# Performance work log

Hardware: AMD Instinct MI355X
Metric: run time of the kernel (lower is better)

## Reference

```python
import jax, jax.numpy as jnp
import numpy as np

N, D, K, P, A = 16384, 256, 32, 64, 5
H, KD, NPT, FACT = 8, 32, 8, 2
RBF_BINS, RBF_MAX, REL_CLIP = 16, 10.0, 32


def _norm(v, eps=1e-6):
    return v * jax.lax.rsqrt(jnp.square(v).sum(-1, keepdims=True) + eps)


def extract_frames(pos):
    # pos: [N, A, 3]; backbone atoms 0=N, 1=CA, 2=C (Gram-Schmidt AF-style frame)
    n, ca, c = pos[:, 0], pos[:, 1], pos[:, 2]
    e1 = _norm(c - ca)
    u = n - ca
    e2 = _norm(u - (u * e1).sum(-1, keepdims=True) * e1)
    e3 = jnp.cross(e1, e2)
    R = jnp.stack([e1, e2, e3], axis=-1)  # [N,3,3], columns = frame axes
    t = ca
    local = jnp.einsum('nji,naj->nai', R, pos - t[:, None])  # R^T (p - t)
    return R, t, local


def distance_rbf(d):
    centers = jnp.linspace(0.0, RBF_MAX, RBF_BINS)
    sigma = RBF_MAX / RBF_BINS
    return jnp.exp(-jnp.square((d[..., None] - centers) / sigma))


def layer_norm(x, scale, offset, eps=1e-5):
    mu = x.mean(-1, keepdims=True)
    var = jnp.square(x - mu).mean(-1, keepdims=True)
    return (x - mu) * jax.lax.rsqrt(var + eps) * scale + offset


def setup_inputs() -> dict:
    key = jax.random.key(0)
    ks = jax.random.split(key, 20)
    f32 = jnp.float32
    rnd = lambda i, shape, s=0.02: jax.random.normal(ks[i], shape, f32) * s
    inp = {}
    inp['local'] = jax.random.normal(ks[0], (N, D), f32)
    inp['pos'] = jax.random.normal(ks[1], (N, A, 3), f32) * 3.0
    inp['neighbours'] = jax.random.randint(ks[2], (N, K), 0, N, jnp.int32)
    inp['resi'] = jnp.arange(N, dtype=jnp.int32) % 512
    inp['chain'] = jnp.arange(N, dtype=jnp.int32) // 2048
    inp['batch'] = jnp.arange(N, dtype=jnp.int32) // 4096
    inp['update_mask'] = jnp.ones((N, 1), bool)
    inp['mask'] = jnp.ones((N,), bool)
    FIN = A * 3 + A * RBF_BINS
    FPAIR = A * 3 + A * RBF_BINS + (2 * REL_CLIP + 1) + 2
    FOUT = H * KD + H * P + H * NPT * 3 + H * NPT
    inp['w_in'] = rnd(3, (FIN, D))
    inp['w_pair'] = rnd(4, (FPAIR, P))
    inp['b_pair'] = jnp.zeros((P,), f32)
    inp['ln1_s'] = jnp.ones((D,), f32); inp['ln1_o'] = jnp.zeros((D,), f32)
    inp['wq'] = rnd(5, (D, H * KD)); inp['wk'] = rnd(6, (D, H * KD)); inp['wv'] = rnd(7, (D, H * KD))
    inp['wqp'] = rnd(8, (D, H * NPT * 3)); inp['wkp'] = rnd(9, (D, H * NPT * 3)); inp['wvp'] = rnd(10, (D, H * NPT * 3))
    inp['wb'] = rnd(11, (P, H))
    inp['gamma'] = jnp.ones((H,), f32)
    inp['wo'] = rnd(12, (FOUT, D)); inp['bo'] = jnp.zeros((D,), f32)
    inp['ln2_s'] = jnp.ones((D,), f32); inp['ln2_o'] = jnp.zeros((D,), f32)
    DH = D * FACT
    inp['wg'] = rnd(13, (D, DH)); inp['wvm'] = rnd(14, (D, DH)); inp['wom'] = rnd(15, (DH, D))
    inp['ln3_s'] = jnp.ones((D,), f32); inp['ln3_o'] = jnp.zeros((D,), f32)
    inp['wpos'] = rnd(16, (D, A * 3))
    return inp


def reference(local, pos, w_in, w_pair, b_pair, ln1_s, ln1_o, wq, wk, wv, wqp, wkp, wvp,
              wb, gamma, wo, bo, ln2_s, ln2_o, wg, wvm, wom, ln3_s, ln3_o, wpos,
              neighbours, resi, chain, batch, update_mask, mask):
    n_res = local.shape[0]
    kk = neighbours.shape[1]
    R, t, local_pos = extract_frames(pos)  # [N,3,3], [N,3], [N,A,3]
    # --- geometric input features ---
    dloc = jnp.sqrt(jnp.square(local_pos).sum(-1) + 1e-12)
    feat = jnp.concatenate([_norm(local_pos).reshape(n_res, -1),
                            distance_rbf(dloc).reshape(n_res, -1)], axis=-1)
    local = local + feat @ w_in
    # --- pair features over kNN edges ---
    idx = jnp.clip(neighbours, 0, n_res - 1)
    pos_j = pos[idx]  # [N,K,A,3]
    rel = jnp.einsum('nji,nkaj->nkai', R, pos_j - t[:, None, None])  # neighbour atoms in frame i
    dij = jnp.sqrt(jnp.square(rel).sum(-1) + 1e-12)  # [N,K,A]
    dirs = rel / (dij[..., None] + 1e-6)
    rp = jnp.clip(resi[idx] - resi[:, None], -REL_CLIP, REL_CLIP) + REL_CLIP
    rp_oh = jax.nn.one_hot(rp, 2 * REL_CLIP + 1, dtype=local.dtype)
    same_chain = (chain[idx] == chain[:, None])[..., None].astype(local.dtype)
    same_batch = (batch[idx] == batch[:, None])[..., None].astype(local.dtype)
    pf = jnp.concatenate([dirs.reshape(n_res, kk, -1), distance_rbf(dij).reshape(n_res, kk, -1),
                          rp_oh, same_chain, same_batch], axis=-1)
    pair = jax.nn.gelu(pf @ w_pair + b_pair)  # [N,K,P]
    pair_mask = mask[:, None] & mask[idx] & (neighbours >= 0) & (batch[idx] == batch[:, None])
    # --- sparse invariant point attention ---
    x = layer_norm(local, ln1_s, ln1_o)
    q = (x @ wq).reshape(n_res, H, KD)
    k = (x @ wk).reshape(n_res, H, KD)
    v = (x @ wv).reshape(n_res, H, KD)
    to_glob = lambda pts: jnp.einsum('nij,nhpj->nhpi', R, pts) + t[:, None, None]
    qp = to_glob((x @ wqp).reshape(n_res, H, NPT, 3))
    kp = to_glob((x @ wkp).reshape(n_res, H, NPT, 3))
    vp = to_glob((x @ wvp).reshape(n_res, H, NPT, 3))
    qk = jnp.einsum('nhd,nkhd->nkh', q, k[idx]) / np.float32(np.sqrt(KD))
    d2 = jnp.square(qp[:, None] - kp[idx]).sum(-1).sum(-1)  # [N,K,H]
    wc = np.float32(np.sqrt(2.0 / (9.0 * NPT)))
    wl = np.float32(np.sqrt(1.0 / 3.0))
    logits = wl * (qk + pair @ wb - 0.5 * wc * jax.nn.softplus(gamma) * d2)
    logits = jnp.where(pair_mask[..., None], logits, -1e9)
    att = jax.nn.softmax(logits, axis=1)
    att = jnp.where(pair_mask[..., None], att, 0.0)
    o_s = jnp.einsum('nkh,nkhd->nhd', att, v[idx]).reshape(n_res, -1)
    o_pt = jnp.einsum('nkh,nkhpi->nhpi', att, vp[idx])
    o_pt = jnp.einsum('nji,nhpj->nhpi', R, o_pt - t[:, None, None])  # back to local frame
    o_n = jnp.sqrt(jnp.square(o_pt).sum(-1) + 1e-8)
    o_pr = jnp.einsum('nkh,nkc->nhc', att, pair).reshape(n_res, -1)
    ipa = jnp.concatenate([o_s, o_pr, o_pt.reshape(n_res, -1), o_n.reshape(n_res, -1)], -1) @ wo + bo
    local = local + ipa
    # --- gated MLP ---
    x = layer_norm(local, ln2_s, ln2_o)
    local = local + (jax.nn.gelu(x @ wg) * (x @ wvm)) @ wom
    # --- equivariant position update (scale = 1.0) ---
    x = layer_norm(local, ln3_s, ln3_o)
    new_lp = local_pos + (x @ wpos).reshape(n_res, A, 3)
    new_pos = jnp.einsum('nij,naj->nai', R, new_lp) + t[:, None]
    pos = jnp.where(update_mask[..., None], new_pos, pos)
    return local, pos
```

## Files before the change

### kernel.cpp

```cpp
#include <hip/hip_runtime.h>
#include <hip/hip_bf16.h>
#include <math.h>

#define DMODEL 256
#define KNB 32
#define NHEAD 8
#define FIN 95
#define FPD 95
#define KPAD 104
#define FOUT 1024
#define DHID 512

typedef __hip_bfloat16 bf16;
typedef __attribute__((ext_vector_type(8))) short short8;
typedef __attribute__((ext_vector_type(4))) float floatx4;

__device__ inline float B2F(bf16 x) { return __bfloat162float(x); }
__device__ inline bf16 F2B(float x) { return __float2bfloat16(x); }
__device__ inline unsigned short f2bs(float x) {
    bf16 h = __float2bfloat16(x);
    return *reinterpret_cast<unsigned short*>(&h);
}
__device__ inline float bs2f(short s) {
    return __uint_as_float(((unsigned)(unsigned short)s) << 16);
}

__device__ inline float gelu_t(float x) {
    return 0.5f * x * (1.f + tanhf(0.7978845608028654f * (x + 0.044715f * x * x * x)));
}

#define OFF_WALL 0
#define OFF_WO   344064
#define OFF_WG   606208
#define OFF_WVM  737280
#define OFF_WOM  868352
#define OFF_WP   999424
#define OFF_WIN  1006080
#define WT_TOTAL 1032704

__global__ __launch_bounds__(256) void kT(const float* __restrict__ wq, const float* __restrict__ wk,
                                          const float* __restrict__ wv, const float* __restrict__ wqp,
                                          const float* __restrict__ wkp, const float* __restrict__ wvp,
                                          const float* __restrict__ wo, const float* __restrict__ wg,
                                          const float* __restrict__ wvm, const float* __restrict__ wom,
                                          const float* __restrict__ w_pair, const float* __restrict__ w_in,
                                          unsigned short* __restrict__ wt) {
    int stride = gridDim.x * 256;
    for (int e = blockIdx.x * 256 + threadIdx.x; e < WT_TOTAL; e += stride) {
        float v;
        if (e < OFF_WO) {
            int n = e >> 8, k = e & 255;
            if (n < 256) v = wq[k * 256 + n];
            else if (n < 512) v = wk[k * 256 + n - 256];
            else if (n < 768) v = wv[k * 256 + n - 512];
            else if (n < 960) v = wqp[k * 192 + n - 768];
            else if (n < 1152) v = wkp[k * 192 + n - 960];
            else v = wvp[k * 192 + n - 1152];
        } else if (e < OFF_WG) {
            int u = e - OFF_WO; int n = u >> 10, k = u & 1023;
            v = wo[k * 256 + n];
        } else if (e < OFF_WVM) {
            int u = e - OFF_WG; int n = u >> 8, k = u & 255;
            v = wg[k * 512 + n];
        } else if (e < OFF_WOM) {
            int u = e - OFF_WVM; int n = u >> 8, k = u & 255;
            v = wvm[k * 512 + n];
        } else if (e < OFF_WP) {
            int u = e - OFF_WOM; int n = u >> 9, k = u & 511;
            v = wom[k * 256 + n];
        } else if (e < OFF_WIN) {
            int u = e - OFF_WP; int n = u / KPAD, k = u % KPAD;
            v = (k < FPD) ? w_pair[k * 64 + n] : 0.f;
        } else {
            int u = e - OFF_WIN; int n = u / KPAD, k = u % KPAD;
            v = (k < FIN) ? w_in[k * 256 + n] : 0.f;
        }
        wt[e] = f2bs(v);
    }
}

__global__ __launch_bounds__(256) void kA1(const float* __restrict__ pos,
                                           float* __restrict__ Rw,
                                           float* __restrict__ lpw,
                                           unsigned short* __restrict__ featb) {
    int tid = threadIdx.x;
    int res = tid >> 5, lt = tid & 31;
    int ri = blockIdx.x * 8 + res;
    const float* pp = pos + (size_t)ri * 15;
    float nx = pp[0], ny = pp[1], nz = pp[2];
    float cax = pp[3], cay = pp[4], caz = pp[5];
    float cx = pp[6], cy = pp[7], cz = pp[8];
    float e1x = cx - cax, e1y = cy - cay, e1z = cz - caz;
    float inv = rsqrtf(e1x * e1x + e1y * e1y + e1z * e1z + 1e-6f);
    e1x *= inv; e1y *= inv; e1z *= inv;
    float ux = nx - cax, uy = ny - cay, uz = nz - caz;
    float d = ux * e1x + uy * e1y + uz * e1z;
    float wx = ux - d * e1x, wy = uy - d * e1y, wz = uz - d * e1z;
    inv = rsqrtf(wx * wx + wy * wy + wz * wz + 1e-6f);
    float e2x = wx * inv, e2y = wy * inv, e2z = wz * inv;
    float e3x = e1y * e2z - e1z * e2y;
    float e3y = e1z * e2x - e1x * e2z;
    float e3z = e1x * e2y - e1y * e2x;
    float R[9] = {e1x, e2x, e3x, e1y, e2y, e3y, e1z, e2z, e3z};

    __shared__ float lpS[8][15];
    __shared__ float ddS[8][5], dinvS[8][5];

    if (lt < 9) Rw[(size_t)ri * 9 + lt] = R[lt];
    if (lt < 15) {
        int a = lt / 3, ii = lt % 3;
        float px = pp[a * 3 + 0] - cax, py = pp[a * 3 + 1] - cay, pz = pp[a * 3 + 2] - caz;
        float v = R[0 * 3 + ii] * px + R[1 * 3 + ii] * py + R[2 * 3 + ii] * pz;
        lpS[res][lt] = v;
        lpw[(size_t)ri * 15 + lt] = v;
    }
    __syncthreads();
    if (lt < 5) {
        float s = lpS[res][lt * 3] * lpS[res][lt * 3] + lpS[res][lt * 3 + 1] * lpS[res][lt * 3 + 1] +
                  lpS[res][lt * 3 + 2] * lpS[res][lt * 3 + 2];
        ddS[res][lt] = sqrtf(s + 1e-12f);
        dinvS[res][lt] = rsqrtf(s + 1e-6f);
    }
    __syncthreads();
    for (int e = lt; e < KPAD; e += 32) {
        float v;
        if (e < 15) v = lpS[res][e] * dinvS[res][e / 3];
        else if (e < 95) {
            int u = e - 15, a = u >> 4, b = u & 15;
            float z = (ddS[res][a] - (float)b * (10.f / 15.f)) * (1.f / 0.625f);
            v = expf(-z * z);
        } else v = 0.f;
        featb[(size_t)ri * KPAD + e] = f2bs(v);
    }
}

__global__ __launch_bounds__(256) void kB(const float* __restrict__ local,
                                          const unsigned short* __restrict__ featb,
                                          const float* __restrict__ ln1_s,
                                          const float* __restrict__ ln1_o,
                                          const unsigned short* __restrict__ wAllT,
                                          const unsigned short* __restrict__ w_inT,
                                          float* __restrict__ dlocal,
                                          bf16* __restrict__ qbh, bf16* __restrict__ kbh,
                                          bf16* __restrict__ vbh, bf16* __restrict__ qpl,
                                          bf16* __restrict__ kpl, bf16* __restrict__ vpl) {
    int r0 = blockIdx.x * 32;
    int tid = threadIdx.x;
    __shared__ __align__(16) unsigned short featA[32 * KPAD];
    __shared__ __align__(16) unsigned short xbf[32 * 264];
    __shared__ float statsS[32 * 4];

    {
        const short8* src = reinterpret_cast<const short8*>(featb + (size_t)r0 * KPAD);
        short8* dst = reinterpret_cast<short8*>(featA);
        for (int c = tid; c < 32 * KPAD / 8; c += 256) dst[c] = src[c];
    }
    __syncthreads();

    int lane = tid & 63, w = tid >> 6;
    int mtile = w & 1, par = w >> 1;
    int m = lane & 15, quad = lane >> 4;

    short8 fa[3];
#pragma unroll
    for (int ks = 0; ks < 3; ks++)
        fa[ks] = *reinterpret_cast<const short8*>(&featA[(mtile * 16 + m) * KPAD + ks * 32 + quad * 8]);
    float lupv[8][4];
#pragma unroll
    for (int j = 0; j < 8; j++) {
        int nt = par + 2 * j;
        floatx4 c = {0.f, 0.f, 0.f, 0.f};
        const short8* bp = reinterpret_cast<const short8*>(w_inT + (size_t)(nt * 16 + m) * KPAD);
#pragma unroll
        for (int ks = 0; ks < 3; ks++)
            c = __builtin_amdgcn_mfma_f32_16x16x32_bf16(fa[ks], bp[ks * 4 + quad], c, 0, 0, 0);
        int col = nt * 16 + m;
#pragma unroll
        for (int r = 0; r < 4; r++) {
            int row = mtile * 16 + quad * 4 + r;
            float lv = local[(size_t)(r0 + row) * 256 + col] + c[r];
            lupv[j][r] = lv;
            dlocal[(size_t)(r0 + row) * 256 + col] = lv;
        }
    }
    {
        float s[4] = {0.f, 0.f, 0.f, 0.f}, ss[4] = {0.f, 0.f, 0.f, 0.f};
#pragma unroll
        for (int j = 0; j < 8; j++)
#pragma unroll
            for (int r = 0; r < 4; r++) { s[r] += lupv[j][r]; ss[r] += lupv[j][r] * lupv[j][r]; }
#pragma unroll
        for (int mask = 1; mask < 16; mask <<= 1)
#pragma unroll
            for (int r = 0; r < 4; r++) { s[r] += __shfl_xor(s[r], mask); ss[r] += __shfl_xor(ss[r], mask); }
        if (m == 0) {
#pragma unroll
            for (int r = 0; r < 4; r++) {
                int row = mtile * 16 + quad * 4 + r;
                statsS[row * 4 + par * 2 + 0] = s[r];
                statsS[row * 4 + par * 2 + 1] = ss[r];
            }
        }
    }
    __syncthreads();
    {
        float mu[4], rs_[4];
#pragma unroll
        for (int r = 0; r < 4; r++) {
            int row = mtile * 16 + quad * 4 + r;
            float S = statsS[row * 4 + 0] + statsS[row * 4 + 2];
            float SS = statsS[row * 4 + 1] + statsS[row * 4 + 3];
            float m_ = S * (1.f / 256.f);
            mu[r] = m_;
            rs_[r] = rsqrtf(SS * (1.f / 256.f) - m_ * m_ + 1e-5f);
        }
#pragma unroll
        for (int j = 0; j < 8; j++) {
            int col = (par + 2 * j) * 16 + m;
            float g = ln1_s[col], o = ln1_o[col];
#pragma unroll
            for (int r = 0; r < 4; r++) {
                int row = mtile * 16 + quad * 4 + r;
                xbf[row * 264 + col] = f2bs((lupv[j][r] - mu[r]) * rs_[r] * g + o);
            }
        }
    }
    __syncthreads();

    short8 afr[8];
#pragma unroll
    for (int ks = 0; ks < 8; ks++)
        afr[ks] = *reinterpret_cast<const short8*>(&xbf[(mtile * 16 + m) * 264 + ks * 32 + quad * 8]);
    for (int nt = par; nt < 84; nt += 2) {
        floatx4 c = {0.f, 0.f, 0.f, 0.f};
        const short8* bp = reinterpret_cast<const short8*>(wAllT + (size_t)(nt * 16 + m) * 256);
#pragma unroll
        for (int ks = 0; ks < 8; ks++)
            c = __builtin_amdgcn_mfma_f32_16x16x32_bf16(afr[ks], bp[ks * 4 + quad], c, 0, 0, 0);
        int colg = nt * 16 + m;
        bf16* O; int c0, ncol;
        if (colg < 256)       { O = qbh; c0 = colg;        ncol = 256; }
        else if (colg < 512)  { O = kbh; c0 = colg - 256;  ncol = 256; }
        else if (colg < 768)  { O = vbh; c0 = colg - 512;  ncol = 256; }
        else if (colg < 960)  { O = qpl; c0 = colg - 768;  ncol = 192; }
        else if (colg < 1152) { O = kpl; c0 = colg - 960;  ncol = 192; }
        else                  { O = vpl; c0 = colg - 1152; ncol = 192; }
#pragma unroll
        for (int r = 0; r < 4; r++) {
            int rg = r0 + mtile * 16 + quad * 4 + r;
            O[(size_t)rg * ncol + c0] = F2B(c[r]);
        }
    }
}

__global__ __launch_bounds__(256) void kP(const bf16* __restrict__ qpl,
                                          const bf16* __restrict__ kpl,
                                          const bf16* __restrict__ vpl,
                                          const float* __restrict__ Rw,
                                          const float* __restrict__ pos,
                                          float* __restrict__ qpg,
                                          float* __restrict__ kpg,
                                          float* __restrict__ vpg) {
    int r0 = blockIdx.x * 4;
    int tid = threadIdx.x;
    for (int u = tid; u < 4 * 192; u += 256) {
        int r = u / 192, e = u % 192, hp = e / 3, ii = e % 3;
        int ri = r0 + r;
        float R0 = Rw[(size_t)ri * 9 + ii * 3 + 0];
        float R1 = Rw[(size_t)ri * 9 + ii * 3 + 1];
        float R2 = Rw[(size_t)ri * 9 + ii * 3 + 2];
        float tt = pos[(size_t)ri * 15 + 3 + ii];
        size_t base = (size_t)ri * 192 + hp * 3;
        qpg[(size_t)ri * 192 + e] = R0 * B2F(qpl[base]) + R1 * B2F(qpl[base + 1]) + R2 * B2F(qpl[base + 2]) + tt;
        kpg[(size_t)ri * 192 + e] = R0 * B2F(kpl[base]) + R1 * B2F(kpl[base + 1]) + R2 * B2F(kpl[base + 2]) + tt;
        vpg[(size_t)ri * 192 + e] = R0 * B2F(vpl[base]) + R1 * B2F(vpl[base + 1]) + R2 * B2F(vpl[base + 2]) + tt;
    }
}

__global__ __launch_bounds__(256) void kC(const float* __restrict__ pos,
                                          const int* __restrict__ nbr,
                                          const int* __restrict__ resi,
                                          const int* __restrict__ chain,
                                          const int* __restrict__ batch,
                                          const int* __restrict__ mask,
                                          const float* __restrict__ Rw,
                                          const float* __restrict__ w_pair,
                                          const unsigned short* __restrict__ wT,
                                          const float* __restrict__ b_pair,
                                          const float* __restrict__ wbm,
                                          const float* __restrict__ gamma,
                                          const bf16* __restrict__ qbh,
                                          const bf16* __restrict__ kbh,
                                          const bf16* __restrict__ vbh,
                                          const float* __restrict__ qpg,
                                          const float* __restrict__ kpg,
                                          const float* __restrict__ vpg,
                                          bf16* __restrict__ ipab,
                                          int N) {
    int i = blockIdx.x;
    int tid = threadIdx.x;
    __shared__ __align__(16) float qS[256];
    __shared__ __align__(16) float qpS[192];
    __shared__ __align__(16) unsigned short pfA[KNB * KPAD];
    __shared__ __align__(16) float pairS[KNB][68];
    __shared__ __align__(16) float wbmS[NHEAD][68];
    __shared__ float lg[KNB * NHEAD];
    __shared__ float optg[192];
    __shared__ float ipaS[FOUT];
    __shared__ int idxS[KNB], rpS[KNB], scS[KNB], sbS[KNB], pmS[KNB];

    float R[9];
#pragma unroll
    for (int u = 0; u < 9; u++) R[u] = Rw[(size_t)i * 9 + u];
    float t0 = pos[(size_t)i * 15 + 3];
    float t1 = pos[(size_t)i * 15 + 4];
    float t2 = pos[(size_t)i * 15 + 5];

    qS[tid] = B2F(qbh[(size_t)i * 256 + tid]);
    if (tid < 192) qpS[tid] = qpg[(size_t)i * 192 + tid];
    if (tid < KNB) {
        int nb = nbr[(size_t)i * KNB + tid];
        int j = min(max(nb, 0), N - 1);
        idxS[tid] = j;
        int rp = resi[j] - resi[i];
        rp = min(max(rp, -32), 32) + 32;
        rpS[tid] = rp;
        scS[tid] = (chain[j] == chain[i]) ? 1 : 0;
        sbS[tid] = (batch[j] == batch[i]) ? 1 : 0;
        pmS[tid] = (mask[i] != 0 && mask[j] != 0 && nb >= 0 && batch[j] == batch[i]) ? 1 : 0;
    }
    __syncthreads();
    for (int u = tid; u < 512; u += 256) {
        int h = u & 7, c = u >> 3;
        wbmS[h][c] = wbm[c * 8 + h];
    }
    if (tid < 160) {
        int kk = tid & 31, a = tid >> 5;
        int j = idxS[kk];
        const float* pj = pos + (size_t)j * 15 + a * 3;
        float px = pj[0] - t0, py = pj[1] - t1, pz = pj[2] - t2;
        float r0_ = R[0] * px + R[3] * py + R[6] * pz;
        float r1_ = R[1] * px + R[4] * py + R[7] * pz;
        float r2_ = R[2] * px + R[5] * py + R[8] * pz;
        float s = r0_ * r0_ + r1_ * r1_ + r2_ * r2_;
        float dij = sqrtf(s + 1e-12f);
        float di = 1.f / (dij + 1e-6f);
        pfA[kk * KPAD + a * 3 + 0] = f2bs(r0_ * di);
        pfA[kk * KPAD + a * 3 + 1] = f2bs(r1_ * di);
        pfA[kk * KPAD + a * 3 + 2] = f2bs(r2_ * di);
        for (int b = 0; b < 16; b++) {
            float z = (dij - (float)b * (10.f / 15.f)) * (1.f / 0.625f);
            pfA[kk * KPAD + 15 + a * 16 + b] = f2bs(expf(-z * z));
        }
    }
    if (tid < KNB) pfA[tid * KPAD + FPD] = 0;
    __syncthreads();

    {
        int lane = tid & 63;
        int wv = tid >> 6;
        int n0 = wv * 16;
        int mrow = lane & 15;
        int quad = lane >> 4;
        floatx4 c0 = {0.f, 0.f, 0.f, 0.f};
        floatx4 c1 = {0.f, 0.f, 0.f, 0.f};
#pragma unroll
        for (int ks = 0; ks < 3; ks++) {
            int k0 = ks * 32 + quad * 8;
            short8 a0 = *reinterpret_cast<const short8*>(&pfA[mrow * KPAD + k0]);
            short8 a1 = *reinterpret_cast<const short8*>(&pfA[(16 + mrow) * KPAD + k0]);
            short8 bb = *reinterpret_cast<const short8*>(&wT[(n0 + mrow) * KPAD + k0]);
            c0 = __builtin_amdgcn_mfma_f32_16x16x32_bf16(a0, bb, c0, 0, 0, 0);
            c1 = __builtin_amdgcn_mfma_f32_16x16x32_bf16(a1, bb, c1, 0, 0, 0);
        }
        int col = n0 + mrow;
        float bp = b_pair[col];
        float w160 = w_pair[160 * 64 + col];
        float w161 = w_pair[161 * 64 + col];
#pragma unroll
        for (int mt = 0; mt < 2; mt++) {
            floatx4 cc = mt ? c1 : c0;
#pragma unroll
            for (int r = 0; r < 4; r++) {
                int row = mt * 16 + quad * 4 + r;
                float s = cc[r] + bp + w_pair[(95 + rpS[row]) * 64 + col] +
                          (scS[row] ? w160 : 0.f) + (sbS[row] ? w161 : 0.f);
                pairS[row][col] = gelu_t(s);
            }
        }
    }
    __syncthreads();

    {
        int kk = tid >> 3, h = tid & 7;
        int j = idxS[kk];
        float qk = 0.f;
        const short8* kj8 = reinterpret_cast<const short8*>(kbh + (size_t)j * 256 + h * 32);
        const floatx4* qh4 = reinterpret_cast<const floatx4*>(qS + h * 32);
#pragma unroll
        for (int e = 0; e < 4; e++) {
            short8 kv = kj8[e];
            floatx4 qa = qh4[2 * e], qb = qh4[2 * e + 1];
            qk += qa[0] * bs2f(kv[0]) + qa[1] * bs2f(kv[1]) + qa[2] * bs2f(kv[2]) + qa[3] * bs2f(kv[3]) +
                  qb[0] * bs2f(kv[4]) + qb[1] * bs2f(kv[5]) + qb[2] * bs2f(kv[6]) + qb[3] * bs2f(kv[7]);
        }
        qk *= 0.17677669529663687f;
        float d2 = 0.f;
        const floatx4* kp4 = reinterpret_cast<const floatx4*>(kpg + (size_t)j * 192 + h * 24);
        const floatx4* qp4 = reinterpret_cast<const floatx4*>(qpS + h * 24);
#pragma unroll
        for (int e = 0; e < 6; e++) {
            floatx4 kv = kp4[e], qv = qp4[e];
#pragma unroll
            for (int q = 0; q < 4; q++) {
                float df = qv[q] - kv[q];
                d2 += df * df;
            }
        }
        float pb = 0.f;
        const floatx4* ps4 = reinterpret_cast<const floatx4*>(&pairS[kk][0]);
        const floatx4* wb4 = reinterpret_cast<const floatx4*>(&wbmS[h][0]);
#pragma unroll
        for (int e = 0; e < 16; e++) {
            floatx4 pv = ps4[e], wv4 = wb4[e];
            pb += pv[0] * wv4[0] + pv[1] * wv4[1] + pv[2] * wv4[2] + pv[3] * wv4[3];
        }
        float sp = log1pf(expf(gamma[h]));
        float lgt = 0.5773502691896258f * (qk + pb - (1.f / 12.f) * sp * d2);
        lg[kk * 8 + h] = pmS[kk] ? lgt : -1e9f;
    }
    __syncthreads();
    if (tid < 8) {
        int h = tid;
        float m = -INFINITY;
        for (int kk = 0; kk < KNB; kk++) m = fmaxf(m, lg[kk * 8 + h]);
        float s = 0.f;
        for (int kk = 0; kk < KNB; kk++) s += expf(lg[kk * 8 + h] - m);
        float invs = 1.f / s;
        for (int kk = 0; kk < KNB; kk++) {
            float a = expf(lg[kk * 8 + h] - m) * invs;
            lg[kk * 8 + h] = pmS[kk] ? a : 0.f;
        }
    }
    __syncthreads();
    {
        int h = tid >> 5, d = tid & 31;
        float s = 0.f;
        for (int kk = 0; kk < KNB; kk++)
            s += lg[kk * 8 + h] * B2F(vbh[(size_t)idxS[kk] * 256 + h * 32 + d]);
        ipaS[h * 32 + d] = s;
    }
    for (int u = tid; u < 512; u += 256) {
        int h = u >> 6, c = u & 63;
        float s = 0.f;
        for (int kk = 0; kk < KNB; kk++) s += lg[kk * 8 + h] * pairS[kk][c];
        ipaS[256 + u] = s;
    }
    if (tid < 192) {
        int h = tid / 24;
        float s = 0.f;
        for (int kk = 0; kk < KNB; kk++)
            s += lg[kk * 8 + h] * vpg[(size_t)idxS[kk] * 192 + tid];
        optg[tid] = s;
    }
    __syncthreads();
    if (tid < 192) {
        int hp = tid / 3, ii = tid % 3;
        float v0 = optg[hp * 3 + 0] - t0, v1 = optg[hp * 3 + 1] - t1, v2 = optg[hp * 3 + 2] - t2;
        ipaS[768 + tid] = R[0 + ii] * v0 + R[3 + ii] * v1 + R[6 + ii] * v2;
    }
    __syncthreads();
    if (tid < 64) {
        float a0 = ipaS[768 + tid * 3], a1 = ipaS[768 + tid * 3 + 1], a2 = ipaS[768 + tid * 3 + 2];
        ipaS[960 + tid] = sqrtf(a0 * a0 + a1 * a1 + a2 * a2 + 1e-8f);
    }
    __syncthreads();
    for (int u = tid; u < FOUT; u += 256) ipab[(size_t)i * FOUT + u] = F2B(ipaS[u]);
}

__global__ __launch_bounds__(256) void kD(const bf16* __restrict__ ipab,
                                          const unsigned short* __restrict__ woT,
                                          const float* __restrict__ bo,
                                          float* __restrict__ dlocal) {
    int r0 = blockIdx.x * 32;
    int tid = threadIdx.x;
    int lane = tid & 63, w = tid >> 6;
    int mtile = w & 1, m = lane & 15, quad = lane >> 4;
    floatx4 acc[8];
#pragma unroll
    for (int j = 0; j < 8; j++) acc[j] = {0.f, 0.f, 0.f, 0.f};
    const short8* arow = reinterpret_cast<const short8*>(ipab + (size_t)(r0 + mtile * 16 + m) * 1024);
    for (int ks = 0; ks < 32; ks++) {
        short8 a = arow[ks * 4 + quad];
#pragma unroll
        for (int j = 0; j < 8; j++) {
            int nt = (w >> 1) + 2 * j;
            const short8* bp = reinterpret_cast<const short8*>(woT + (size_t)(nt * 16 + m) * 1024);
            acc[j] = __builtin_amdgcn_mfma_f32_16x16x32_bf16(a, bp[ks * 4 + quad], acc[j], 0, 0, 0);
        }
    }
#pragma unroll
    for (int j = 0; j < 8; j++) {
        int nt = (w >> 1) + 2 * j;
        int colg = nt * 16 + m;
        float bov = bo[colg];
#pragma unroll
        for (int r = 0; r < 4; r++) {
            size_t off = (size_t)(r0 + mtile * 16 + quad * 4 + r) * 256 + colg;
            dlocal[off] += acc[j][r] + bov;
        }
    }
}

__global__ __launch_bounds__(256) void kE(const float* __restrict__ ln2_s,
                                          const float* __restrict__ ln2_o,
                                          const unsigned short* __restrict__ wgT,
                                          const unsigned short* __restrict__ wvmT,
                                          const unsigned short* __restrict__ womT,
                                          float* __restrict__ dlocal) {
    int r0 = blockIdx.x * 32;
    int tid = threadIdx.x;
    __shared__ __align__(16) unsigned short xbf[32 * 264];
    __shared__ __align__(16) unsigned short hbf[32 * 520];
    {
        int row = tid >> 3, seg = tid & 7;
        const floatx4* src = reinterpret_cast<const floatx4*>(dlocal + (size_t)(r0 + row) * 256 + seg * 32);
        floatx4 vv[8];
        float s = 0.f, ss = 0.f;
#pragma unroll
        for (int e = 0; e < 8; e++) {
            vv[e] = src[e];
#pragma unroll
            for (int q = 0; q < 4; q++) { s += vv[e][q]; ss += vv[e][q] * vv[e][q]; }
        }
        s += __shfl_xor(s, 1); ss += __shfl_xor(ss, 1);
        s += __shfl_xor(s, 2); ss += __shfl_xor(ss, 2);
        s += __shfl_xor(s, 4); ss += __shfl_xor(ss, 4);
        float mu = s * (1.f / 256.f);
        float var = ss * (1.f / 256.f) - mu * mu;
        float rs = rsqrtf(var + 1e-5f);
#pragma unroll
        for (int e = 0; e < 8; e++) {
#pragma unroll
            for (int q = 0; q < 4; q++) {
                int f = seg * 32 + e * 4 + q;
                xbf[row * 264 + f] = f2bs((vv[e][q] - mu) * rs * ln2_s[f] + ln2_o[f]);
            }
        }
    }
    __syncthreads();
    int lane = tid & 63, w = tid >> 6;
    int mtile = w & 1, m = lane & 15, quad = lane >> 4;
    short8 afr[8];
#pragma unroll
    for (int ks = 0; ks < 8; ks++)
        afr[ks] = *reinterpret_cast<const short8*>(&xbf[(mtile * 16 + m) * 264 + ks * 32 + quad * 8]);
    for (int nt = (w >> 1); nt < 32; nt += 2) {
        floatx4 cg = {0.f, 0.f, 0.f, 0.f};
        floatx4 cv = {0.f, 0.f, 0.f, 0.f};
        const short8* bg = reinterpret_cast<const short8*>(wgT + (size_t)(nt * 16 + m) * 256);
        const short8* bv = reinterpret_cast<const short8*>(wvmT + (size_t)(nt * 16 + m) * 256);
#pragma unroll
        for (int ks = 0; ks < 8; ks++) {
            cg = __builtin_amdgcn_mfma_f32_16x16x32_bf16(afr[ks], bg[ks * 4 + quad], cg, 0, 0, 0);
            cv = __builtin_amdgcn_mfma_f32_16x16x32_bf16(afr[ks], bv[ks * 4 + quad], cv, 0, 0, 0);
        }
#pragma unroll
        for (int r = 0; r < 4; r++) {
            int row = mtile * 16 + quad * 4 + r;
            hbf[row * 520 + nt * 16 + m] = f2bs(gelu_t(cg[r]) * cv[r]);
        }
    }
    __syncthreads();
    floatx4 acc[8];
#pragma unroll
    for (int j = 0; j < 8; j++) acc[j] = {0.f, 0.f, 0.f, 0.f};
    for (int ks = 0; ks < 16; ks++) {
        short8 a = *reinterpret_cast<const short8*>(&hbf[(mtile * 16 + m) * 520 + ks * 32 + quad * 8]);
#pragma unroll
        for (int j = 0; j < 8; j++) {
            int nt = (w >> 1) + 2 * j;
            const short8* bp = reinterpret_cast<const short8*>(womT + (size_t)(nt * 16 + m) * 512);
            acc[j] = __builtin_amdgcn_mfma_f32_16x16x32_bf16(a, bp[ks * 4 + quad], acc[j], 0, 0, 0);
        }
    }
#pragma unroll
    for (int j = 0; j < 8; j++) {
        int nt = (w >> 1) + 2 * j;
        int colg = nt * 16 + m;
#pragma unroll
        for (int r = 0; r < 4; r++) {
            size_t off = (size_t)(r0 + mtile * 16 + quad * 4 + r) * 256 + colg;
            dlocal[off] += acc[j][r];
        }
    }
}

__global__ __launch_bounds__(256) void kF(const float* __restrict__ dlocal,
                                          const float* __restrict__ ln3_s,
                                          const float* __restrict__ ln3_o,
                                          const float* __restrict__ wpos,
                                          const float* __restrict__ lpw,
                                          const float* __restrict__ Rw,
                                          const float* __restrict__ pos,
                                          const int* __restrict__ umask,
                                          float* __restrict__ outp) {
    int tid = threadIdx.x;
    int r = tid >> 5, lt = tid & 31;
    int ri = blockIdx.x * 8 + r;
    __shared__ float x3S[8][256];
    __shared__ float nlS[8][15];
    {
        const floatx4* src = reinterpret_cast<const floatx4*>(dlocal + (size_t)ri * 256 + lt * 8);
        floatx4 v0 = src[0], v1 = src[1];
        float s = 0.f, ss = 0.f;
#pragma unroll
        for (int q = 0; q < 4; q++) {
            s += v0[q] + v1[q];
            ss += v0[q] * v0[q] + v1[q] * v1[q];
        }
#pragma unroll
        for (int mask = 1; mask < 32; mask <<= 1) { s += __shfl_xor(s, mask); ss += __shfl_xor(ss, mask); }
        float mu = s * (1.f / 256.f);
        float var = ss * (1.f / 256.f) - mu * mu;
        float rs = rsqrtf(var + 1e-5f);
#pragma unroll
        for (int q = 0; q < 4; q++) {
            int f0 = lt * 8 + q, f1 = lt * 8 + 4 + q;
            x3S[r][f0] = (v0[q] - mu) * rs * ln3_s[f0] + ln3_o[f0];
            x3S[r][f1] = (v1[q] - mu) * rs * ln3_s[f1] + ln3_o[f1];
        }
    }
    __syncthreads();
    {
        int g = tid >> 5, sub = tid & 31;
        for (int out = g; out < 120; out += 8) {
            int rr = out / 15, e = out % 15;
            float partial = 0.f;
#pragma unroll
            for (int i2 = 0; i2 < 8; i2++) {
                int f = sub + 32 * i2;
                partial += x3S[rr][f] * wpos[f * 15 + e];
            }
#pragma unroll
            for (int mask = 1; mask < 32; mask <<= 1) partial += __shfl_xor(partial, mask);
            if (sub == 0) nlS[rr][e] = lpw[(size_t)(blockIdx.x * 8 + rr) * 15 + e] + partial;
        }
    }
    __syncthreads();
    if (tid < 120) {
        int rr = tid / 15, e = tid % 15;
        int rj = blockIdx.x * 8 + rr;
        int a2 = e / 3, ii = e % 3;
        float R0 = Rw[(size_t)rj * 9 + ii * 3 + 0];
        float R1 = Rw[(size_t)rj * 9 + ii * 3 + 1];
        float R2 = Rw[(size_t)rj * 9 + ii * 3 + 2];
        float tt = pos[(size_t)rj * 15 + 3 + ii];
        float np = R0 * nlS[rr][a2 * 3 + 0] + R1 * nlS[rr][a2 * 3 + 1] + R2 * nlS[rr][a2 * 3 + 2] + tt;
        float old = pos[(size_t)rj * 15 + e];
        outp[(size_t)rj * 15 + e] = (umask[rj] != 0) ? np : old;
    }
}

extern "C" void kernel_launch(void* const* d_in, const int* in_sizes, int n_in,
                              void* d_out, int out_size, void* d_ws, size_t ws_size,
                              hipStream_t stream) {
    static const int map_dict[31] = {0, 1, 2, 3, 4, 5, 6, 7, 8, 9, 10, 11, 12, 13, 14, 15,
                                     16, 17, 18, 19, 20, 21, 22, 23, 24, 25, 26, 27, 28, 29, 30};
    static const int map_sig[31] = {0, 1, 25, 26, 27, 28, 29, 30, 2, 3, 4, 5, 6, 7, 8, 9,
                                    10, 11, 12, 13, 14, 15, 16, 17, 18, 19, 20, 21, 22, 23, 24};
    const int* M = (in_sizes[2] == FIN * DMODEL) ? map_sig : map_dict;

    const float* local = (const float*)d_in[M[0]];
    const float* pos = (const float*)d_in[M[1]];
    const int* nbr = (const int*)d_in[M[2]];
    const int* resi = (const int*)d_in[M[3]];
    const int* chain = (const int*)d_in[M[4]];
    const int* batch = (const int*)d_in[M[5]];
    const int* umask = (const int*)d_in[M[6]];
    const int* mask = (const int*)d_in[M[7]];
    const float* w_in = (const float*)d_in[M[8]];
    const float* w_pair = (const float*)d_in[M[9]];
    const float* b_pair = (const float*)d_in[M[10]];
    const float* ln1_s = (const float*)d_in[M[11]];
    const float* ln1_o = (const float*)d_in[M[12]];
    const float* wq = (const float*)d_in[M[13]];
    const float* wk = (const float*)d_in[M[14]];
    const float* wv = (const float*)d_in[M[15]];
    const float* wqp = (const float*)d_in[M[16]];
    const float* wkp = (const float*)d_in[M[17]];
    const float* wvp = (const float*)d_in[M[18]];
    const float* wbm = (const float*)d_in[M[19]];
    const float* gamma = (const float*)d_in[M[20]];
    const float* wo = (const float*)d_in[M[21]];
    const float* bo = (const float*)d_in[M[22]];
    const float* ln2_s = (const float*)d_in[M[23]];
    const float* ln2_o = (const float*)d_in[M[24]];
    const float* wg = (const float*)d_in[M[25]];
    const float* wvm = (const float*)d_in[M[26]];
    const float* wom = (const float*)d_in[M[27]];
    const float* ln3_s = (const float*)d_in[M[28]];
    const float* ln3_o = (const float*)d_in[M[29]];
    const float* wpos = (const float*)d_in[M[30]];

    int N = in_sizes[0] / DMODEL;

    float* out_local = (float*)d_out;
    float* out_pos = out_local + (size_t)N * DMODEL;

    char* wsb = (char*)d_ws;
    float* Rw = (float*)wsb;   wsb += (size_t)N * 9 * 4;
    float* lpw = (float*)wsb;  wsb += (size_t)N * 15 * 4;
    bf16* qbh = (bf16*)wsb;    wsb += (size_t)N * 256 * 2;
    bf16* kbh = (bf16*)wsb;    wsb += (size_t)N * 256 * 2;
    bf16* vbh = (bf16*)wsb;    wsb += (size_t)N * 256 * 2;
    bf16* qpl = (bf16*)wsb;    wsb += (size_t)N * 192 * 2;
    bf16* kpl = (bf16*)wsb;    wsb += (size_t)N * 192 * 2;
    bf16* vpl = (bf16*)wsb;    wsb += (size_t)N * 192 * 2;
    bf16* ipab = (bf16*)wsb;   wsb += (size_t)N * 1024 * 2;
    float* qpg = (float*)wsb;  wsb += (size_t)N * 192 * 4;
    float* kpg = (float*)wsb;  wsb += (size_t)N * 192 * 4;
    float* vpg = (float*)wsb;  wsb += (size_t)N * 192 * 4;
    unsigned short* featb = (unsigned short*)wsb; wsb += (size_t)N * KPAD * 2;
    unsigned short* wtrans = (unsigned short*)wsb; wsb += (size_t)WT_TOTAL * 2;
    unsigned short* wAllT = wtrans + OFF_WALL;
    unsigned short* woT   = wtrans + OFF_WO;
    unsigned short* wgT   = wtrans + OFF_WG;
    unsigned short* wvmT  = wtrans + OFF_WVM;
    unsigned short* womT  = wtrans + OFF_WOM;
    unsigned short* wpT   = wtrans + OFF_WP;
    unsigned short* winT  = wtrans + OFF_WIN;

    dim3 blk(256);
    hipLaunchKernelGGL(kT, dim3(512), blk, 0, stream, wq, wk, wv, wqp, wkp, wvp,
                       wo, wg, wvm, wom, w_pair, w_in, wtrans);
    hipLaunchKernelGGL(kA1, dim3(N / 8), blk, 0, stream, pos, Rw, lpw, featb);
    hipLaunchKernelGGL(kB, dim3(N / 32), blk, 0, stream, local, featb, ln1_s, ln1_o, wAllT, winT,
                       out_local, qbh, kbh, vbh, qpl, kpl, vpl);
    hipLaunchKernelGGL(kP, dim3(N / 4), blk, 0, stream, qpl, kpl, vpl, Rw, pos, qpg, kpg, vpg);
    hipLaunchKernelGGL(kC, dim3(N), blk, 0, stream, pos, nbr, resi, chain, batch, mask, Rw,
                       w_pair, wpT, b_pair, wbm, gamma, qbh, kbh, vbh, qpg, kpg, vpg, ipab, N);
    hipLaunchKernelGGL(kD, dim3(N / 32), blk, 0, stream, ipab, woT, bo, out_local);
    hipLaunchKernelGGL(kE, dim3(N / 32), blk, 0, stream, ln2_s, ln2_o, wgT, wvmT, womT, out_local);
    hipLaunchKernelGGL(kF, dim3(N / 8), blk, 0, stream, out_local, ln3_s, ln3_o, wpos, lpw, Rw, pos,
                       umask, out_pos);
}
```

Baseline: 731.7 us.

## Fuse output projection with gated MLP and interleave K/V gather buffers

Merges the IPA output projection and the gated-MLP kernels into one kernel. The residual stays in registers and the layer norm is computed from MFMA accumulators with cross-lane shuffles, which removes a global round trip of the residual stream and one launch. K and V (scalar and point) are now stored interleaved per residue, so the neighbour gathers in the attention kernel hit one contiguous region per row. The softplus of gamma is precomputed once per block, and the per-head softmax is spread over 64 threads with shuffle reductions instead of 8 serial threads. The fused kernel keeps more accumulators live, which may raise register pressure.

```diff
diff --git a/kernel.cpp b/kernel.cpp
--- a/kernel.cpp
+++ b/kernel.cpp
@@ -141,9 +141,9 @@
                                           const unsigned short* __restrict__ wAllT,
                                           const unsigned short* __restrict__ w_inT,
                                           float* __restrict__ dlocal,
-                                          bf16* __restrict__ qbh, bf16* __restrict__ kbh,
-                                          bf16* __restrict__ vbh, bf16* __restrict__ qpl,
-                                          bf16* __restrict__ kpl, bf16* __restrict__ vpl) {
+                                          bf16* __restrict__ qbh, bf16* __restrict__ kvb,
+                                          bf16* __restrict__ qpl, bf16* __restrict__ kpl,
+                                          bf16* __restrict__ vpl) {
     int r0 = blockIdx.x * 32;
     int tid = threadIdx.x;
     __shared__ __align__(16) unsigned short featA[32 * KPAD];
@@ -240,8 +240,7 @@
         int colg = nt * 16 + m;
         bf16* O; int c0, ncol;
         if (colg < 256)       { O = qbh; c0 = colg;        ncol = 256; }
-        else if (colg < 512)  { O = kbh; c0 = colg - 256;  ncol = 256; }
-        else if (colg < 768)  { O = vbh; c0 = colg - 512;  ncol = 256; }
+        else if (colg < 768)  { O = kvb; c0 = colg - 256;  ncol = 512; }
         else if (colg < 960)  { O = qpl; c0 = colg - 768;  ncol = 192; }
         else if (colg < 1152) { O = kpl; c0 = colg - 960;  ncol = 192; }
         else                  { O = vpl; c0 = colg - 1152; ncol = 192; }
@@ -259,8 +258,7 @@
                                           const float* __restrict__ Rw,
                                           const float* __restrict__ pos,
                                           float* __restrict__ qpg,
-                                          float* __restrict__ kpg,
-                                          float* __restrict__ vpg) {
+                                          float* __restrict__ kvpg) {
     int r0 = blockIdx.x * 4;
     int tid = threadIdx.x;
     for (int u = tid; u < 4 * 192; u += 256) {
@@ -272,8 +270,8 @@
         float tt = pos[(size_t)ri * 15 + 3 + ii];
         size_t base = (size_t)ri * 192 + hp * 3;
         qpg[(size_t)ri * 192 + e] = R0 * B2F(qpl[base]) + R1 * B2F(qpl[base + 1]) + R2 * B2F(qpl[base + 2]) + tt;
-        kpg[(size_t)ri * 192 + e] = R0 * B2F(kpl[base]) + R1 * B2F(kpl[base + 1]) + R2 * B2F(kpl[base + 2]) + tt;
-        vpg[(size_t)ri * 192 + e] = R0 * B2F(vpl[base]) + R1 * B2F(vpl[base + 1]) + R2 * B2F(vpl[base + 2]) + tt;
+        kvpg[(size_t)ri * 384 + e] = R0 * B2F(kpl[base]) + R1 * B2F(kpl[base + 1]) + R2 * B2F(kpl[base + 2]) + tt;
+        kvpg[(size_t)ri * 384 + 192 + e] = R0 * B2F(vpl[base]) + R1 * B2F(vpl[base + 1]) + R2 * B2F(vpl[base + 2]) + tt;
     }
 }
 
@@ -290,11 +288,9 @@
                                           const float* __restrict__ wbm,
                                           const float* __restrict__ gamma,
                                           const bf16* __restrict__ qbh,
-                                          const bf16* __restrict__ kbh,
-                                          const bf16* __restrict__ vbh,
+                                          const bf16* __restrict__ kvb,
                                           const float* __restrict__ qpg,
-                                          const float* __restrict__ kpg,
-                                          const float* __restrict__ vpg,
+                                          const float* __restrict__ kvpg,
                                           bf16* __restrict__ ipab,
                                           int N) {
     int i = blockIdx.x;
@@ -304,6 +300,7 @@
     __shared__ __align__(16) unsigned short pfA[KNB * KPAD];
     __shared__ __align__(16) float pairS[KNB][68];
     __shared__ __align__(16) float wbmS[NHEAD][68];
+    __shared__ float spS[NHEAD];
     __shared__ float lg[KNB * NHEAD];
     __shared__ float optg[192];
     __shared__ float ipaS[FOUT];
@@ -334,6 +331,7 @@
         int h = u & 7, c = u >> 3;
         wbmS[h][c] = wbm[c * 8 + h];
     }
+    if (tid >= 192 && tid < 200) spS[tid - 192] = log1pf(expf(gamma[tid - 192]));
     if (tid < 160) {
         int kk = tid & 31, a = tid >> 5;
         int j = idxS[kk];
@@ -395,7 +393,7 @@
         int kk = tid >> 3, h = tid & 7;
         int j = idxS[kk];
         float qk = 0.f;
-        const short8* kj8 = reinterpret_cast<const short8*>(kbh + (size_t)j * 256 + h * 32);
+        const short8* kj8 = reinterpret_cast<const short8*>(kvb + (size_t)j * 512 + h * 32);
         const floatx4* qh4 = reinterpret_cast<const floatx4*>(qS + h * 32);
 #pragma unroll
         for (int e = 0; e < 4; e++) {
@@ -406,7 +404,7 @@
         }
         qk *= 0.17677669529663687f;
         float d2 = 0.f;
-        const floatx4* kp4 = reinterpret_cast<const floatx4*>(kpg + (size_t)j * 192 + h * 24);
+        const floatx4* kp4 = reinterpret_cast<const floatx4*>(kvpg + (size_t)j * 384 + h * 24);
         const floatx4* qp4 = reinterpret_cast<const floatx4*>(qpS + h * 24);
 #pragma unroll
         for (int e = 0; e < 6; e++) {
@@ -425,21 +423,31 @@
             floatx4 pv = ps4[e], wv4 = wb4[e];
             pb += pv[0] * wv4[0] + pv[1] * wv4[1] + pv[2] * wv4[2] + pv[3] * wv4[3];
         }
-        float sp = log1pf(expf(gamma[h]));
-        float lgt = 0.5773502691896258f * (qk + pb - (1.f / 12.f) * sp * d2);
+        float lgt = 0.5773502691896258f * (qk + pb - (1.f / 12.f) * spS[h] * d2);
         lg[kk * 8 + h] = pmS[kk] ? lgt : -1e9f;
     }
     __syncthreads();
-    if (tid < 8) {
-        int h = tid;
+    if (tid < 64) {
+        int h = tid >> 3, sub = tid & 7;
         float m = -INFINITY;
-        for (int kk = 0; kk < KNB; kk++) m = fmaxf(m, lg[kk * 8 + h]);
-        float s = 0.f;
-        for (int kk = 0; kk < KNB; kk++) s += expf(lg[kk * 8 + h] - m);
+        float lv[4];
+#pragma unroll
+        for (int q = 0; q < 4; q++) {
+            lv[q] = lg[(sub + 8 * q) * 8 + h];
+            m = fmaxf(m, lv[q]);
+        }
+#pragma unroll
+        for (int mk = 1; mk < 8; mk <<= 1) m = fmaxf(m, __shfl_xor(m, mk));
+        float s = 0.f, ex[4];
+#pragma unroll
+        for (int q = 0; q < 4; q++) { ex[q] = expf(lv[q] - m); s += ex[q]; }
+#pragma unroll
+        for (int mk = 1; mk < 8; mk <<= 1) s += __shfl_xor(s, mk);
         float invs = 1.f / s;
-        for (int kk = 0; kk < KNB; kk++) {
-            float a = expf(lg[kk * 8 + h] - m) * invs;
-            lg[kk * 8 + h] = pmS[kk] ? a : 0.f;
+#pragma unroll
+        for (int q = 0; q < 4; q++) {
+            int kk = sub + 8 * q;
+            lg[kk * 8 + h] = pmS[kk] ? ex[q] * invs : 0.f;
         }
     }
     __syncthreads();
@@ -447,7 +455,7 @@
         int h = tid >> 5, d = tid & 31;
         float s = 0.f;
         for (int kk = 0; kk < KNB; kk++)
-            s += lg[kk * 8 + h] * B2F(vbh[(size_t)idxS[kk] * 256 + h * 32 + d]);
+            s += lg[kk * 8 + h] * B2F(kvb[(size_t)idxS[kk] * 512 + 256 + h * 32 + d]);
         ipaS[h * 32 + d] = s;
     }
     for (int u = tid; u < 512; u += 256) {
@@ -460,7 +468,7 @@
         int h = tid / 24;
         float s = 0.f;
         for (int kk = 0; kk < KNB; kk++)
-            s += lg[kk * 8 + h] * vpg[(size_t)idxS[kk] * 192 + tid];
+            s += lg[kk * 8 + h] * kvpg[(size_t)idxS[kk] * 384 + 192 + tid];
         optg[tid] = s;
     }
     __syncthreads();
@@ -478,84 +486,94 @@
     for (int u = tid; u < FOUT; u += 256) ipab[(size_t)i * FOUT + u] = F2B(ipaS[u]);
 }
 
-__global__ __launch_bounds__(256) void kD(const bf16* __restrict__ ipab,
-                                          const unsigned short* __restrict__ woT,
-                                          const float* __restrict__ bo,
-                                          float* __restrict__ dlocal) {
-    int r0 = blockIdx.x * 32;
-    int tid = threadIdx.x;
-    int lane = tid & 63, w = tid >> 6;
-    int mtile = w & 1, m = lane & 15, quad = lane >> 4;
-    floatx4 acc[8];
-#pragma unroll
-    for (int j = 0; j < 8; j++) acc[j] = {0.f, 0.f, 0.f, 0.f};
-    const short8* arow = reinterpret_cast<const short8*>(ipab + (size_t)(r0 + mtile * 16 + m) * 1024);
-    for (int ks = 0; ks < 32; ks++) {
-        short8 a = arow[ks * 4 + quad];
-#pragma unroll
-        for (int j = 0; j < 8; j++) {
-            int nt = (w >> 1) + 2 * j;
-            const short8* bp = reinterpret_cast<const short8*>(woT + (size_t)(nt * 16 + m) * 1024);
-            acc[j] = __builtin_amdgcn_mfma_f32_16x16x32_bf16(a, bp[ks * 4 + quad], acc[j], 0, 0, 0);
-        }
-    }
-#pragma unroll
-    for (int j = 0; j < 8; j++) {
-        int nt = (w >> 1) + 2 * j;
-        int colg = nt * 16 + m;
-        float bov = bo[colg];
-#pragma unroll
-        for (int r = 0; r < 4; r++) {
-            size_t off = (size_t)(r0 + mtile * 16 + quad * 4 + r) * 256 + colg;
-            dlocal[off] += acc[j][r] + bov;
-        }
-    }
-}
-
-__global__ __launch_bounds__(256) void kE(const float* __restrict__ ln2_s,
-                                          const float* __restrict__ ln2_o,
-                                          const unsigned short* __restrict__ wgT,
-                                          const unsigned short* __restrict__ wvmT,
-                                          const unsigned short* __restrict__ womT,
-                                          float* __restrict__ dlocal) {
+__global__ __launch_bounds__(256) void kDE(const bf16* __restrict__ ipab,
+                                           const unsigned short* __restrict__ woT,
+                                           const float* __restrict__ bo,
+                                           const float* __restrict__ ln2_s,
+                                           const float* __restrict__ ln2_o,
+                                           const unsigned short* __restrict__ wgT,
+                                           const unsigned short* __restrict__ wvmT,
+                                           const unsigned short* __restrict__ womT,
+                                           float* __restrict__ dlocal) {
     int r0 = blockIdx.x * 32;
     int tid = threadIdx.x;
     __shared__ __align__(16) unsigned short xbf[32 * 264];
     __shared__ __align__(16) unsigned short hbf[32 * 520];
-    {
-        int row = tid >> 3, seg = tid & 7;
-        const floatx4* src = reinterpret_cast<const floatx4*>(dlocal + (size_t)(r0 + row) * 256 + seg * 32);
-        floatx4 vv[8];
-        float s = 0.f, ss = 0.f;
-#pragma unroll
-        for (int e = 0; e < 8; e++) {
-            vv[e] = src[e];
-#pragma unroll
-            for (int q = 0; q < 4; q++) { s += vv[e][q]; ss += vv[e][q] * vv[e][q]; }
-        }
-        s += __shfl_xor(s, 1); ss += __shfl_xor(ss, 1);
-        s += __shfl_xor(s, 2); ss += __shfl_xor(ss, 2);
-        s += __shfl_xor(s, 4); ss += __shfl_xor(ss, 4);
-        float mu = s * (1.f / 256.f);
-        float var = ss * (1.f / 256.f) - mu * mu;
-        float rs = rsqrtf(var + 1e-5f);
-#pragma unroll
-        for (int e = 0; e < 8; e++) {
-#pragma unroll
-            for (int q = 0; q < 4; q++) {
-                int f = seg * 32 + e * 4 + q;
-                xbf[row * 264 + f] = f2bs((vv[e][q] - mu) * rs * ln2_s[f] + ln2_o[f]);
+    __shared__ float statsS[32 * 4];
+    int lane = tid & 63, w = tid >> 6;
+    int mtile = w & 1, par = w >> 1, m = lane & 15, quad = lane >> 4;
+
+    floatx4 l2[8];
+#pragma unroll
+    for (int j = 0; j < 8; j++) l2[j] = {0.f, 0.f, 0.f, 0.f};
+    const short8* arow = reinterpret_cast<const short8*>(ipab + (size_t)(r0 + mtile * 16 + m) * 1024);
+    for (int ks = 0; ks < 32; ks++) {
+        short8 a = arow[ks * 4 + quad];
+#pragma unroll
+        for (int j = 0; j < 8; j++) {
+            int nt = par + 2 * j;
+            const short8* bp = reinterpret_cast<const short8*>(woT + (size_t)(nt * 16 + m) * 1024);
+            l2[j] = __builtin_amdgcn_mfma_f32_16x16x32_bf16(a, bp[ks * 4 + quad], l2[j], 0, 0, 0);
+        }
+    }
+#pragma unroll
+    for (int j = 0; j < 8; j++) {
+        int colg = (par + 2 * j) * 16 + m;
+        float bov = bo[colg];
+#pragma unroll
+        for (int r = 0; r < 4; r++) {
+            int row = mtile * 16 + quad * 4 + r;
+            l2[j][r] += dlocal[(size_t)(r0 + row) * 256 + colg] + bov;
+        }
+    }
+    {
+        float s[4] = {0.f, 0.f, 0.f, 0.f}, ss[4] = {0.f, 0.f, 0.f, 0.f};
+#pragma unroll
+        for (int j = 0; j < 8; j++)
+#pragma unroll
+            for (int r = 0; r < 4; r++) { s[r] += l2[j][r]; ss[r] += l2[j][r] * l2[j][r]; }
+#pragma unroll
+        for (int mask = 1; mask < 16; mask <<= 1)
+#pragma unroll
+            for (int r = 0; r < 4; r++) { s[r] += __shfl_xor(s[r], mask); ss[r] += __shfl_xor(ss[r], mask); }
+        if (m == 0) {
+#pragma unroll
+            for (int r = 0; r < 4; r++) {
+                int row = mtile * 16 + quad * 4 + r;
+                statsS[row * 4 + par * 2 + 0] = s[r];
+                statsS[row * 4 + par * 2 + 1] = ss[r];
             }
         }
     }
     __syncthreads();
-    int lane = tid & 63, w = tid >> 6;
-    int mtile = w & 1, m = lane & 15, quad = lane >> 4;
+    {
+        float mu[4], rs_[4];
+#pragma unroll
+        for (int r = 0; r < 4; r++) {
+            int row = mtile * 16 + quad * 4 + r;
+            float S = statsS[row * 4 + 0] + statsS[row * 4 + 2];
+            float SS = statsS[row * 4 + 1] + statsS[row * 4 + 3];
+            float m_ = S * (1.f / 256.f);
+            mu[r] = m_;
+            rs_[r] = rsqrtf(SS * (1.f / 256.f) - m_ * m_ + 1e-5f);
+        }
+#pragma unroll
+        for (int j = 0; j < 8; j++) {
+            int colg = (par + 2 * j) * 16 + m;
+            float g = ln2_s[colg], o = ln2_o[colg];
+#pragma unroll
+            for (int r = 0; r < 4; r++) {
+                int row = mtile * 16 + quad * 4 + r;
+                xbf[row * 264 + colg] = f2bs((l2[j][r] - mu[r]) * rs_[r] * g + o);
+            }
+        }
+    }
+    __syncthreads();
     short8 afr[8];
 #pragma unroll
     for (int ks = 0; ks < 8; ks++)
         afr[ks] = *reinterpret_cast<const short8*>(&xbf[(mtile * 16 + m) * 264 + ks * 32 + quad * 8]);
-    for (int nt = (w >> 1); nt < 32; nt += 2) {
+    for (int nt = par; nt < 32; nt += 2) {
         floatx4 cg = {0.f, 0.f, 0.f, 0.f};
         floatx4 cv = {0.f, 0.f, 0.f, 0.f};
         const short8* bg = reinterpret_cast<const short8*>(wgT + (size_t)(nt * 16 + m) * 256);
@@ -579,19 +597,18 @@
         short8 a = *reinterpret_cast<const short8*>(&hbf[(mtile * 16 + m) * 520 + ks * 32 + quad * 8]);
 #pragma unroll
         for (int j = 0; j < 8; j++) {
-            int nt = (w >> 1) + 2 * j;
+            int nt = par + 2 * j;
             const short8* bp = reinterpret_cast<const short8*>(womT + (size_t)(nt * 16 + m) * 512);
             acc[j] = __builtin_amdgcn_mfma_f32_16x16x32_bf16(a, bp[ks * 4 + quad], acc[j], 0, 0, 0);
         }
     }
 #pragma unroll
     for (int j = 0; j < 8; j++) {
-        int nt = (w >> 1) + 2 * j;
-        int colg = nt * 16 + m;
+        int colg = (par + 2 * j) * 16 + m;
 #pragma unroll
         for (int r = 0; r < 4; r++) {
-            size_t off = (size_t)(r0 + mtile * 16 + quad * 4 + r) * 256 + colg;
-            dlocal[off] += acc[j][r];
+            int row = mtile * 16 + quad * 4 + r;
+            dlocal[(size_t)(r0 + row) * 256 + colg] = l2[j][r] + acc[j][r];
         }
     }
 }
@@ -712,15 +729,13 @@
     float* Rw = (float*)wsb;   wsb += (size_t)N * 9 * 4;
     float* lpw = (float*)wsb;  wsb += (size_t)N * 15 * 4;
     bf16* qbh = (bf16*)wsb;    wsb += (size_t)N * 256 * 2;
-    bf16* kbh = (bf16*)wsb;    wsb += (size_t)N * 256 * 2;
-    bf16* vbh = (bf16*)wsb;    wsb += (size_t)N * 256 * 2;
+    bf16* kvb = (bf16*)wsb;    wsb += (size_t)N * 512 * 2;
     bf16* qpl = (bf16*)wsb;    wsb += (size_t)N * 192 * 2;
     bf16* kpl = (bf16*)wsb;    wsb += (size_t)N * 192 * 2;
     bf16* vpl = (bf16*)wsb;    wsb += (size_t)N * 192 * 2;
     bf16* ipab = (bf16*)wsb;   wsb += (size_t)N * 1024 * 2;
     float* qpg = (float*)wsb;  wsb += (size_t)N * 192 * 4;
-    float* kpg = (float*)wsb;  wsb += (size_t)N * 192 * 4;
-    float* vpg = (float*)wsb;  wsb += (size_t)N * 192 * 4;
+    float* kvpg = (float*)wsb; wsb += (size_t)N * 384 * 4;
     unsigned short* featb = (unsigned short*)wsb; wsb += (size_t)N * KPAD * 2;
     unsigned short* wtrans = (unsigned short*)wsb; wsb += (size_t)WT_TOTAL * 2;
     unsigned short* wAllT = wtrans + OFF_WALL;
@@ -736,12 +751,12 @@
                        wo, wg, wvm, wom, w_pair, w_in, wtrans);
     hipLaunchKernelGGL(kA1, dim3(N / 8), blk, 0, stream, pos, Rw, lpw, featb);
     hipLaunchKernelGGL(kB, dim3(N / 32), blk, 0, stream, local, featb, ln1_s, ln1_o, wAllT, winT,
-                       out_local, qbh, kbh, vbh, qpl, kpl, vpl);
-    hipLaunchKernelGGL(kP, dim3(N / 4), blk, 0, stream, qpl, kpl, vpl, Rw, pos, qpg, kpg, vpg);
+                       out_local, qbh, kvb, qpl, kpl, vpl);
+    hipLaunchKernelGGL(kP, dim3(N / 4), blk, 0, stream, qpl, kpl, vpl, Rw, pos, qpg, kvpg);
     hipLaunchKernelGGL(kC, dim3(N), blk, 0, stream, pos, nbr, resi, chain, batch, mask, Rw,
-                       w_pair, wpT, b_pair, wbm, gamma, qbh, kbh, vbh, qpg, kpg, vpg, ipab, N);
-    hipLaunchKernelGGL(kD, dim3(N / 32), blk, 0, stream, ipab, woT, bo, out_local);
-    hipLaunchKernelGGL(kE, dim3(N / 32), blk, 0, stream, ln2_s, ln2_o, wgT, wvmT, womT, out_local);
+                       w_pair, wpT, b_pair, wbm, gamma, qbh, kvb, qpg, kvpg, ipab, N);
+    hipLaunchKernelGGL(kDE, dim3(N / 32), blk, 0, stream, ipab, woT, bo, ln2_s, ln2_o,
+                       wgT, wvmT, womT, out_local);
     hipLaunchKernelGGL(kF, dim3(N / 8), blk, 0, stream, out_local, ln3_s, ln3_o, wpos, lpw, Rw, pos,
                        umask, out_pos);
 }
```

After: 669.8 us. 1.09x faster.
